# Kernel optimization log

Measured on AMD Instinct MI355X. Metric: run time of the kernel, lower is better.

## Reference

```python
import jax, jax.numpy as jnp
import numpy as np
from jax import lax

K = 3; KK = K * K; S = 1; P = 1; D = 1
BN_EPS = 1e-5


def setup_inputs() -> dict:
    key = jax.random.key(0)
    ks = jax.random.split(key, 4)
    B, C, H, W = 8, 128, 64, 64
    cout = 128
    # xavier-ish scales for conv weights
    def xavier(k, shape):
        fan_in = shape[1] * shape[2] * shape[3]
        fan_out = shape[0] * shape[2] * shape[3]
        limit = np.sqrt(6.0 / (fan_in + fan_out))
        return jax.random.uniform(k, shape, jnp.float32, -limit, limit)
    return {
        "x": jax.random.normal(ks[0], (B, C, H, W), jnp.float32),
        "w_off": xavier(ks[1], (2 * KK, C, K, K)),
        "b_off": jnp.zeros((2 * KK,), jnp.float32),
        "w_mod": xavier(ks[2], (KK, C, K, K)),
        "b_mod": jnp.zeros((KK,), jnp.float32),
        "w_reg": xavier(ks[3], (cout, C, K, K)),
        "b_reg": jnp.zeros((cout,), jnp.float32),
        "gamma": jnp.ones((cout,), jnp.float32),
        "beta": jnp.zeros((cout,), jnp.float32),
    }


def _conv(x, w, b):
    y = lax.conv_general_dilated(x, w, (S, S), [(P, P), (P, P)],
                                 rhs_dilation=(D, D),
                                 dimension_numbers=("NCHW", "OIHW", "NCHW"))
    return y + b[None, :, None, None]


def _deform_conv(x, offset, mask, w_reg, b_reg):
    B, C, H, W = x.shape
    Ho, Wo = offset.shape[2], offset.shape[3]
    # torchvision layout: [B, 2*KK, Ho, Wo], interleaved (dy, dx) per tap
    off = offset.reshape(B, KK, 2, Ho, Wo)
    dy, dx = off[:, :, 0], off[:, :, 1]                      # [B,KK,Ho,Wo]
    ki = jnp.arange(KK) // K
    kj = jnp.arange(KK) % K
    base_y = (jnp.arange(Ho) * S - P)[None, :, None] + (ki * D)[:, None, None]  # [KK,Ho,1]
    base_x = (jnp.arange(Wo) * S - P)[None, None, :] + (kj * D)[:, None, None]  # [KK,1,Wo]
    py = base_y[None].astype(x.dtype) + dy                   # [B,KK,Ho,Wo]
    px = base_x[None].astype(x.dtype) + dx

    y0f = jnp.floor(py); x0f = jnp.floor(px)
    ly = py - y0f; lx = px - x0f
    y0 = y0f.astype(jnp.int32); x0 = x0f.astype(jnp.int32)
    y1 = y0 + 1; x1 = x0 + 1

    def gather(iy, ix):
        valid = ((iy >= 0) & (iy < H) & (ix >= 0) & (ix < W)).astype(x.dtype)
        iyc = jnp.clip(iy, 0, H - 1)
        ixc = jnp.clip(ix, 0, W - 1)
        v = jax.vmap(lambda img, a, b: img[:, a, b])(x, iyc, ixc)  # [B,C,KK,Ho,Wo]
        return v * valid[:, None]

    val = (gather(y0, x0) * ((1 - ly) * (1 - lx))[:, None]
           + gather(y0, x1) * ((1 - ly) * lx)[:, None]
           + gather(y1, x0) * (ly * (1 - lx))[:, None]
           + gather(y1, x1) * (ly * lx)[:, None])               # [B,C,KK,Ho,Wo]

    patches = val * mask[:, None]                               # modulated samples
    wr = w_reg.reshape(w_reg.shape[0], C, KK)
    out = jnp.einsum("ock,bckhw->bohw", wr, patches)
    return out + b_reg[None, :, None, None]


def reference(x, w_off, b_off, w_mod, b_mod, w_reg, b_reg, gamma, beta):
    offset = _conv(x, w_off, b_off)
    modulator = 2.0 * jax.nn.sigmoid(_conv(x, w_mod, b_mod))
    y = _deform_conv(x, offset, modulator, w_reg, b_reg)
    # BatchNorm2d (training-mode batch statistics) + ReLU
    mu = y.mean(axis=(0, 2, 3), keepdims=True)
    var = y.var(axis=(0, 2, 3), keepdims=True)
    y = (y - mu) * lax.rsqrt(var + BN_EPS)
    y = y * gamma[None, :, None, None] + beta[None, :, None, None]
    return jax.nn.relu(y)
```

## Files before the change

### kernel.cpp

```cpp
#include <hip/hip_runtime.h>
#include <math.h>

#define H 64
#define W 64
#define C 128
#define NB 8
#define COUT 128
#define HWi 4096
#define NKC 36
#define PADu 40

typedef __attribute__((ext_vector_type(8))) short short8;
typedef __attribute__((ext_vector_type(8))) unsigned short ushort8;
typedef __attribute__((ext_vector_type(4))) unsigned short ushort4v;
typedef __attribute__((ext_vector_type(4))) float f32x4;

__device__ __forceinline__ unsigned short f2bf(float f){
    unsigned u = __float_as_uint(f);
    unsigned r = (u + 0x7FFFu + ((u >> 16) & 1u)) >> 16;
    return (unsigned short)r;
}
__device__ __forceinline__ float bf2f(unsigned short u){
    return __uint_as_float(((unsigned)u) << 16);
}

__global__ void k_pre(const float* __restrict__ x, unsigned short* __restrict__ xTp,
                      const float* __restrict__ w_reg, const float* __restrict__ w_off,
                      const float* __restrict__ w_mod, const float* __restrict__ b_off,
                      const float* __restrict__ b_mod,
                      unsigned short* __restrict__ wAv, unsigned short* __restrict__ w27A,
                      float* __restrict__ biasom, float* __restrict__ psum){
    int tid = threadIdx.x;
    if (blockIdx.x >= 528){
        int i = (blockIdx.x - 528) * 256 + tid;
        if (i < 147456){
            int kc = i >> 12, rem = i & 4095;
            int q = rem >> 10, r = (rem >> 3) & 127, j = rem & 7;
            int kk = kc * 32 + q * 8 + j, k = kk >> 7, c = kk & 127;
            wAv[i] = f2bf(w_reg[r * 1152 + c * 9 + k]);
        } else if (i < 147456 + 36864){
            int j2 = i - 147456;
            int kc = j2 >> 10, rem = j2 & 1023, m = rem >> 5, kkl = rem & 31;
            int kk = kc * 32 + kkl, k = kk >> 7, c = kk & 127;
            float v = 0.f;
            if (m < 18) v = w_off[m * 1152 + c * 9 + k];
            else if (m < 27) v = w_mod[(m - 18) * 1152 + c * 9 + k];
            w27A[j2] = f2bf(v);
        } else if (i < 147456 + 36864 + 32){
            int m = i - 147456 - 36864;
            biasom[m] = (m < 18) ? b_off[m] : (m < 27 ? b_mod[m - 18] : 0.f);
        } else if (i < 147456 + 36864 + 32 + 256){
            psum[i - 147456 - 36864 - 32] = 0.f;
        }
        return;
    }
    int bidx = blockIdx.x;
    int b = bidx & 7, hp = bidx >> 3;
    unsigned short* row = xTp + (size_t)(b * 66 + hp) * 66 * 128;
    if (hp == 0 || hp == 65){
        ushort8 z = {0,0,0,0,0,0,0,0};
        for (int i = tid; i < 66 * 128 / 8; i += 256) ((ushort8*)row)[i] = z;
        return;
    }
    int h = hp - 1;
    __shared__ unsigned short s[64 * 136];
    int w = tid & 63, c0 = tid >> 6;
    for (int cc = 0; cc < 128; cc += 4){
        int c = cc + c0;
        s[w * 136 + c] = f2bf(x[(size_t)(b * 128 + c) * HWi + h * 64 + w]);
    }
    __syncthreads();
    if (tid < 32){
        ushort8 z = {0,0,0,0,0,0,0,0};
        int wp = (tid < 16) ? 0 : 65;
        int sg = tid & 15;
        *(ushort8*)(row + wp * 128 + sg * 8) = z;
    }
    for (int it = tid; it < 1024; it += 256){
        int w2 = it >> 4, sg = it & 15;
        *(ushort8*)(row + (w2 + 1) * 128 + sg * 8) = *(const ushort8*)(s + w2 * 136 + sg * 8);
    }
}

__global__ __launch_bounds__(512, 4) void k_fused(const unsigned short* __restrict__ xTp,
        const unsigned short* __restrict__ w27A, const float* __restrict__ biasom,
        const unsigned short* __restrict__ wAv, const float* __restrict__ b_reg,
        unsigned short* __restrict__ ybf, float* __restrict__ psum){
    __shared__ char smem[79872];
    int tid = threadIdx.x;
    int lb = (blockIdx.x & 7) * 64 + (blockIdx.x >> 3);
    int n0 = lb * 64;
    int b = n0 >> 12, h = (n0 >> 6) & 63;

    {
        int grp = tid >> 8, gt = tid & 255;
        unsigned short* pA = (unsigned short*)(smem + grp * 15360);
        unsigned short* pB = (unsigned short*)(smem + grp * 15360 + 5120);
        int wvg = gt >> 6, lane = gt & 63, quad = lane >> 4, l16 = lane & 15;
        int nl = gt >> 2, sg = gt & 3;
        f32x4 acc0 = {0.f,0.f,0.f,0.f}, acc1 = {0.f,0.f,0.f,0.f};
        int kc0 = grp * 18;
        auto p1load = [&](int i, ushort8& A8, ushort8& B8){
            int kc = kc0 + i;
            int k = kc >> 2, cb = (kc & 3) << 5;
            int ki = k / 3, kj = k - ki * 3;
            if (gt < 128) A8 = *(const ushort8*)(w27A + kc * 1024 + gt * 8);
            int rowi = (b * 66 + h + ki) * 66 + (nl + kj);
            B8 = *(const ushort8*)(xTp + (size_t)rowi * 128 + cb + sg * 8);
        };
        auto p1body = [&](int i, ushort8& A8, ushort8& B8){
            int p = i & 1;
            if (gt < 128) *(ushort8*)(pA + p * 1280 + (gt >> 2) * PADu + (gt & 3) * 8) = A8;
            *(ushort8*)(pB + p * 2560 + nl * PADu + sg * 8) = B8;
            if (i + 2 < 18) p1load(i + 2, A8, B8);
            __syncthreads();
            short8 bfrag = *(const short8*)(pB + p * 2560 + (wvg * 16 + l16) * PADu + quad * 8);
            short8 a0 = *(const short8*)(pA + p * 1280 + l16 * PADu + quad * 8);
            short8 a1 = *(const short8*)(pA + p * 1280 + (16 + l16) * PADu + quad * 8);
            acc0 = __builtin_amdgcn_mfma_f32_16x16x32_bf16(a0, bfrag, acc0, 0, 0, 0);
            acc1 = __builtin_amdgcn_mfma_f32_16x16x32_bf16(a1, bfrag, acc1, 0, 0, 0);
        };
        ushort8 rA0, rB0, rA1, rB1;
        p1load(0, rA0, rB0);
        p1load(1, rA1, rB1);
        for (int ih = 0; ih < 9; ih++){
            p1body(ih * 2,     rA0, rB0);
            p1body(ih * 2 + 1, rA1, rB1);
        }
        float* s_red = (float*)(smem + 30720);
        int npx = wvg * 16 + l16;
        if (grp == 1){
            #pragma unroll
            for (int t = 0; t < 2; t++){
                f32x4 a = t ? acc1 : acc0;
                #pragma unroll
                for (int r = 0; r < 4; r++)
                    s_red[npx * 32 + t * 16 + quad * 4 + r] = a[r];
            }
        }
        __syncthreads();
        if (grp == 0){
            unsigned short* s_OM = (unsigned short*)smem;
            #pragma unroll
            for (int t = 0; t < 2; t++){
                f32x4 a = t ? acc1 : acc0;
                #pragma unroll
                for (int r = 0; r < 4; r++){
                    int oc = t * 16 + quad * 4 + r;
                    float v = a[r] + s_red[npx * 32 + oc] + biasom[oc];
                    if (oc >= 18) v = 2.f / (1.f + expf(-v));
                    s_OM[npx * 32 + oc] = f2bf(v);
                }
            }
        }
        __syncthreads();
    }

    unsigned short* sA = (unsigned short*)smem;
    unsigned short* sB = (unsigned short*)(smem + 40960);
    int*   s_a0 = (int*)(smem + 61440);
    float* s_w0 = (float*)(smem + 70656);
    const unsigned short* s_OM = (const unsigned short*)smem;

    for (int idx = tid; idx < 576; idx += 512){
        int k = idx >> 6, px_ = idx & 63;
        float dy = bf2f(s_OM[px_ * 32 + 2 * k]);
        float dx = bf2f(s_OM[px_ * 32 + 2 * k + 1]);
        float m  = bf2f(s_OM[px_ * 32 + 18 + k]);
        int ki = k / 3, kj = k - ki * 3;
        float py  = (float)(h - 1 + ki) + dy;
        float pxf = (float)(px_ - 1 + kj) + dx;
        float y0f = floorf(py), x0f = floorf(pxf);
        float ly = py - y0f, lx = pxf - x0f;
        int iy0 = (int)y0f, ix0 = (int)x0f;
        int cy0 = min(max(iy0 + 1, 0), 65), cy1 = min(max(iy0 + 2, 0), 65);
        int cx0 = min(max(ix0 + 1, 0), 65), cx1 = min(max(ix0 + 2, 0), 65);
        int rb = b * 66 * 66;
        s_a0[0 * 576 + idx] = ((rb + cy0 * 66) + cx0) * 128;
        s_a0[1 * 576 + idx] = ((rb + cy0 * 66) + cx1) * 128;
        s_a0[2 * 576 + idx] = ((rb + cy1 * 66) + cx0) * 128;
        s_a0[3 * 576 + idx] = ((rb + cy1 * 66) + cx1) * 128;
        s_w0[0 * 576 + idx] = (1.f - ly) * (1.f - lx) * m;
        s_w0[1 * 576 + idx] = (1.f - ly) * lx * m;
        s_w0[2 * 576 + idx] = ly * (1.f - lx) * m;
        s_w0[3 * 576 + idx] = ly * lx * m;
    }
    __syncthreads();

    int wv = tid >> 6, lane = tid & 63, quad = lane >> 4, l16 = lane & 15;
    int ocq = wv & 3, ng = wv >> 2;
    int rA = tid & 127, qA = tid >> 7;
    int cA = (qA ^ ((rA >> 3) & 3)) * 8;
    int px = tid >> 3, cg = tid & 7;

    int rowA0 = ocq * 32 + l16, rowA1 = rowA0 + 16;
    int offA0 = rowA0 * PADu + (quad ^ ((rowA0 >> 3) & 3)) * 8;
    int offA1 = rowA1 * PADu + (quad ^ ((rowA1 >> 3) & 3)) * 8;
    int offB0 = (ng * 32 + l16) * PADu + quad * 8;
    int offB1 = (ng * 32 + 16 + l16) * PADu + quad * 8;

    f32x4 acc00 = {0.f,0.f,0.f,0.f}, acc01 = {0.f,0.f,0.f,0.f};
    f32x4 acc10 = {0.f,0.f,0.f,0.f}, acc11 = {0.f,0.f,0.f,0.f};

    auto loadP = [&](int j, ushort8& W0, ushort8& W1, ushort8& C0, ushort8& C1,
                     ushort8& C2, ushort8& C3, float4& Wt){
        W0 = *(const ushort8*)(wAv + (size_t)(2 * j) * 4096 + tid * 8);
        W1 = *(const ushort8*)(wAv + (size_t)(2 * j + 1) * 4096 + tid * 8);
        int k = j >> 1, cb = (j & 1) << 6;
        int idx = k * 64 + px;
        int co = cb + cg * 8;
        Wt.x = s_w0[0 * 576 + idx]; Wt.y = s_w0[1 * 576 + idx];
        Wt.z = s_w0[2 * 576 + idx]; Wt.w = s_w0[3 * 576 + idx];
        C0 = *(const ushort8*)(xTp + s_a0[0 * 576 + idx] + co);
        C1 = *(const ushort8*)(xTp + s_a0[1 * 576 + idx] + co);
        C2 = *(const ushort8*)(xTp + s_a0[2 * 576 + idx] + co);
        C3 = *(const ushort8*)(xTp + s_a0[3 * 576 + idx] + co);
    };
    auto bodyP = [&](int j, ushort8& W0, ushort8& W1, ushort8& C0, ushort8& C1,
                     ushort8& C2, ushort8& C3, float4& Wt){
        int p = j & 1;
        unsigned short* sAp = sA + p * 10240;
        unsigned short* sBp = sB + p * 5120;
        *(ushort8*)(sAp + rA * PADu + cA) = W0;
        *(ushort8*)(sAp + 5120 + rA * PADu + cA) = W1;
        {
            ushort8 o;
            #pragma unroll
            for (int s = 0; s < 8; s++){
                float v = Wt.x * bf2f(C0[s]) + Wt.y * bf2f(C1[s])
                        + Wt.z * bf2f(C2[s]) + Wt.w * bf2f(C3[s]);
                o[s] = f2bf(v);
            }
            *(ushort8*)(sBp + (cg >> 2) * 2560 + px * PADu + (cg & 3) * 8) = o;
        }
        if (j + 2 < 18) loadP(j + 2, W0, W1, C0, C1, C2, C3, Wt);
        __syncthreads();
        #pragma unroll
        for (int u = 0; u < 2; u++){
            const unsigned short* A = sAp + u * 5120;
            const unsigned short* Bn = sBp + u * 2560;
            short8 a0 = *(const short8*)(A + offA0);
            short8 a1 = *(const short8*)(A + offA1);
            short8 b0 = *(const short8*)(Bn + offB0);
            short8 b1 = *(const short8*)(Bn + offB1);
            acc00 = __builtin_amdgcn_mfma_f32_16x16x32_bf16(a0, b0, acc00, 0, 0, 0);
            acc01 = __builtin_amdgcn_mfma_f32_16x16x32_bf16(a0, b1, acc01, 0, 0, 0);
            acc10 = __builtin_amdgcn_mfma_f32_16x16x32_bf16(a1, b0, acc10, 0, 0, 0);
            acc11 = __builtin_amdgcn_mfma_f32_16x16x32_bf16(a1, b1, acc11, 0, 0, 0);
        }
    };

    ushort8 W0a, W1a, C0a, C1a, C2a, C3a, W0b, W1b, C0b, C1b, C2b, C3b;
    float4 Wta, Wtb;
    loadP(0, W0a, W1a, C0a, C1a, C2a, C3a, Wta);
    loadP(1, W0b, W1b, C0b, C1b, C2b, C3b, Wtb);
    for (int jh = 0; jh < 9; jh++){
        bodyP(jh * 2,     W0a, W1a, C0a, C1a, C2a, C3a, Wta);
        bodyP(jh * 2 + 1, W0b, W1b, C0b, C1b, C2b, C3b, Wtb);
    }

    __syncthreads();
    float* ls = (float*)smem;
    int sp0 = h * 64;
    #pragma unroll
    for (int to = 0; to < 2; to++){
        #pragma unroll
        for (int tn = 0; tn < 2; tn++){
            f32x4 a = to ? (tn ? acc11 : acc10) : (tn ? acc01 : acc00);
            int nl = ng * 32 + tn * 16 + l16;
            #pragma unroll
            for (int r = 0; r < 4; r++){
                int oc = ocq * 32 + to * 16 + quad * 4 + r;
                float v = a[r] + b_reg[oc];
                ybf[(size_t)(b * 128 + oc) * HWi + sp0 + nl] = f2bf(v);
                ls[oc * 67 + nl] = v;
            }
        }
    }
    __syncthreads();
    if (tid < 128){
        int oc = tid;
        float s = 0.f, s2 = 0.f;
        #pragma unroll 8
        for (int nl = 0; nl < 64; nl++){
            float v = ls[oc * 67 + nl];
            s += v; s2 = fmaf(v, v, s2);
        }
        atomicAdd(&psum[oc], s);
        atomicAdd(&psum[128 + oc], s2);
    }
}

__global__ void k_apply(const unsigned short* __restrict__ ybf, const float* __restrict__ psum,
                        const float* __restrict__ gamma, const float* __restrict__ beta,
                        float* __restrict__ out){
    int lb = ((int)blockIdx.x & 7) * 256 + ((int)blockIdx.x >> 3);
    int e8 = (lb * 256 + (int)threadIdx.x) * 8;
    int c = (e8 >> 12) & 127;
    ushort8 u = *(const ushort8*)(ybf + e8);
    float s = psum[c], s2 = psum[128 + c];
    float mean = s * (1.f / 32768.f);
    float var  = s2 * (1.f / 32768.f) - mean * mean;
    float rs = rsqrtf(var + 1e-5f);
    float g = gamma[c] * rs;
    float bt = beta[c] - mean * g;
    float4 lo, hi;
    lo.x = fmaxf(fmaf(bf2f(u[0]), g, bt), 0.f);
    lo.y = fmaxf(fmaf(bf2f(u[1]), g, bt), 0.f);
    lo.z = fmaxf(fmaf(bf2f(u[2]), g, bt), 0.f);
    lo.w = fmaxf(fmaf(bf2f(u[3]), g, bt), 0.f);
    hi.x = fmaxf(fmaf(bf2f(u[4]), g, bt), 0.f);
    hi.y = fmaxf(fmaf(bf2f(u[5]), g, bt), 0.f);
    hi.z = fmaxf(fmaf(bf2f(u[6]), g, bt), 0.f);
    hi.w = fmaxf(fmaf(bf2f(u[7]), g, bt), 0.f);
    *(float4*)(out + e8)     = lo;
    *(float4*)(out + e8 + 4) = hi;
}

extern "C" void kernel_launch(void* const* d_in, const int* in_sizes, int n_in,
                              void* d_out, int out_size, void* d_ws, size_t ws_size,
                              hipStream_t stream){
    const float* x     = (const float*)d_in[0];
    const float* w_off = (const float*)d_in[1];
    const float* b_off = (const float*)d_in[2];
    const float* w_mod = (const float*)d_in[3];
    const float* b_mod = (const float*)d_in[4];
    const float* w_reg = (const float*)d_in[5];
    const float* b_reg = (const float*)d_in[6];
    const float* gamma = (const float*)d_in[7];
    const float* beta  = (const float*)d_in[8];

    char* wsb = (char*)d_ws;
    unsigned short* xTp   = (unsigned short*)(wsb);
    unsigned short* ybf   = (unsigned short*)(wsb + 11018240);
    unsigned short* wAv   = (unsigned short*)(wsb + 19406848);
    unsigned short* w27A  = (unsigned short*)(wsb + 19701760);
    float*          biasom= (float*)(wsb + 19775488);
    float*          psum  = (float*)(wsb + 19775616);
    float* out = (float*)d_out;

    hipLaunchKernelGGL(k_pre,   dim3(1250), dim3(256), 0, stream, x, xTp, w_reg, w_off, w_mod, b_off, b_mod, wAv, w27A, biasom, psum);
    hipLaunchKernelGGL(k_fused, dim3(512),  dim3(512), 0, stream, xTp, w27A, biasom, wAv, b_reg, ybf, psum);
    hipLaunchKernelGGL(k_apply, dim3(2048), dim3(256), 0, stream, ybf, psum, gamma, beta, out);
}
```

Measured before the change: 132.4 us.

## Load MFMA weight fragments directly from global, dropping LDS staging for weights

Both GEMM phases now read their A-operand weight fragments straight from global memory into registers, with the weight pre-layout changed so each lane's fragment is contiguous. This removes the LDS round trip for weights and cuts shared memory from about 78KB to 38KB, which could allow more resident blocks. The bf16 packing of the bilinear samples now uses the hardware v_cvt_pk_bf16_f32 instruction. In exchange, weight loads happen every iteration with global latency that is no longer prefetched two stages ahead, and these loads rely on L2/L1 hits since every block re-reads the weights.

```diff
diff --git a/kernel.cpp b/kernel.cpp
--- a/kernel.cpp
+++ b/kernel.cpp
@@ -12,7 +12,7 @@
 
 typedef __attribute__((ext_vector_type(8))) short short8;
 typedef __attribute__((ext_vector_type(8))) unsigned short ushort8;
-typedef __attribute__((ext_vector_type(4))) unsigned short ushort4v;
+typedef __attribute__((ext_vector_type(4))) unsigned int uint4v;
 typedef __attribute__((ext_vector_type(4))) float f32x4;
 
 __device__ __forceinline__ unsigned short f2bf(float f){
@@ -22,6 +22,11 @@
 }
 __device__ __forceinline__ float bf2f(unsigned short u){
     return __uint_as_float(((unsigned)u) << 16);
+}
+__device__ __forceinline__ unsigned cvtpk_bf16(float lo, float hi){
+    unsigned r;
+    asm("v_cvt_pk_bf16_f32 %0, %1, %2" : "=v"(r) : "v"(lo), "v"(hi));
+    return r;
 }
 
 __global__ void k_pre(const float* __restrict__ x, unsigned short* __restrict__ xTp,
@@ -40,7 +45,9 @@
             wAv[i] = f2bf(w_reg[r * 1152 + c * 9 + k]);
         } else if (i < 147456 + 36864){
             int j2 = i - 147456;
-            int kc = j2 >> 10, rem = j2 & 1023, m = rem >> 5, kkl = rem & 31;
+            int kc = j2 >> 10, rem = j2 & 1023;
+            int q = rem >> 8, m = (rem >> 3) & 31, t = rem & 7;
+            int kkl = q * 8 + t;
             int kk = kc * 32 + kkl, k = kk >> 7, c = kk & 127;
             float v = 0.f;
             if (m < 18) v = w_off[m * 1152 + c * 9 + k];
@@ -86,7 +93,7 @@
         const unsigned short* __restrict__ w27A, const float* __restrict__ biasom,
         const unsigned short* __restrict__ wAv, const float* __restrict__ b_reg,
         unsigned short* __restrict__ ybf, float* __restrict__ psum){
-    __shared__ char smem[79872];
+    __shared__ char smem[38912];
     int tid = threadIdx.x;
     int lb = (blockIdx.x & 7) * 64 + (blockIdx.x >> 3);
     int n0 = lb * 64;
@@ -94,40 +101,39 @@
 
     {
         int grp = tid >> 8, gt = tid & 255;
-        unsigned short* pA = (unsigned short*)(smem + grp * 15360);
-        unsigned short* pB = (unsigned short*)(smem + grp * 15360 + 5120);
+        unsigned short* pB = (unsigned short*)(smem + grp * 10240);
         int wvg = gt >> 6, lane = gt & 63, quad = lane >> 4, l16 = lane & 15;
         int nl = gt >> 2, sg = gt & 3;
         f32x4 acc0 = {0.f,0.f,0.f,0.f}, acc1 = {0.f,0.f,0.f,0.f};
         int kc0 = grp * 18;
-        auto p1load = [&](int i, ushort8& A8, ushort8& B8){
+        auto p1load = [&](int i, ushort8& B8){
             int kc = kc0 + i;
             int k = kc >> 2, cb = (kc & 3) << 5;
             int ki = k / 3, kj = k - ki * 3;
-            if (gt < 128) A8 = *(const ushort8*)(w27A + kc * 1024 + gt * 8);
             int rowi = (b * 66 + h + ki) * 66 + (nl + kj);
             B8 = *(const ushort8*)(xTp + (size_t)rowi * 128 + cb + sg * 8);
         };
-        auto p1body = [&](int i, ushort8& A8, ushort8& B8){
+        auto p1body = [&](int i, ushort8& B8){
             int p = i & 1;
-            if (gt < 128) *(ushort8*)(pA + p * 1280 + (gt >> 2) * PADu + (gt & 3) * 8) = A8;
+            int kc = kc0 + i;
+            const unsigned short* wj = w27A + kc * 1024 + quad * 256;
+            short8 a0 = *(const short8*)(wj + l16 * 8);
+            short8 a1 = *(const short8*)(wj + (16 + l16) * 8);
             *(ushort8*)(pB + p * 2560 + nl * PADu + sg * 8) = B8;
-            if (i + 2 < 18) p1load(i + 2, A8, B8);
+            if (i + 2 < 18) p1load(i + 2, B8);
             __syncthreads();
             short8 bfrag = *(const short8*)(pB + p * 2560 + (wvg * 16 + l16) * PADu + quad * 8);
-            short8 a0 = *(const short8*)(pA + p * 1280 + l16 * PADu + quad * 8);
-            short8 a1 = *(const short8*)(pA + p * 1280 + (16 + l16) * PADu + quad * 8);
             acc0 = __builtin_amdgcn_mfma_f32_16x16x32_bf16(a0, bfrag, acc0, 0, 0, 0);
             acc1 = __builtin_amdgcn_mfma_f32_16x16x32_bf16(a1, bfrag, acc1, 0, 0, 0);
         };
-        ushort8 rA0, rB0, rA1, rB1;
-        p1load(0, rA0, rB0);
-        p1load(1, rA1, rB1);
+        ushort8 rB0, rB1;
+        p1load(0, rB0);
+        p1load(1, rB1);
         for (int ih = 0; ih < 9; ih++){
-            p1body(ih * 2,     rA0, rB0);
-            p1body(ih * 2 + 1, rA1, rB1);
-        }
-        float* s_red = (float*)(smem + 30720);
+            p1body(ih * 2,     rB0);
+            p1body(ih * 2 + 1, rB1);
+        }
+        float* s_red = (float*)(smem + 20480);
         int npx = wvg * 16 + l16;
         if (grp == 1){
             #pragma unroll
@@ -156,10 +162,9 @@
         __syncthreads();
     }
 
-    unsigned short* sA = (unsigned short*)smem;
-    unsigned short* sB = (unsigned short*)(smem + 40960);
-    int*   s_a0 = (int*)(smem + 61440);
-    float* s_w0 = (float*)(smem + 70656);
+    unsigned short* sB = (unsigned short*)smem;
+    int*   s_a0 = (int*)(smem + 20480);
+    float* s_w0 = (float*)(smem + 29696);
     const unsigned short* s_OM = (const unsigned short*)smem;
 
     for (int idx = tid; idx < 576; idx += 512){
@@ -189,23 +194,16 @@
 
     int wv = tid >> 6, lane = tid & 63, quad = lane >> 4, l16 = lane & 15;
     int ocq = wv & 3, ng = wv >> 2;
-    int rA = tid & 127, qA = tid >> 7;
-    int cA = (qA ^ ((rA >> 3) & 3)) * 8;
     int px = tid >> 3, cg = tid & 7;
 
     int rowA0 = ocq * 32 + l16, rowA1 = rowA0 + 16;
-    int offA0 = rowA0 * PADu + (quad ^ ((rowA0 >> 3) & 3)) * 8;
-    int offA1 = rowA1 * PADu + (quad ^ ((rowA1 >> 3) & 3)) * 8;
     int offB0 = (ng * 32 + l16) * PADu + quad * 8;
     int offB1 = (ng * 32 + 16 + l16) * PADu + quad * 8;
 
     f32x4 acc00 = {0.f,0.f,0.f,0.f}, acc01 = {0.f,0.f,0.f,0.f};
     f32x4 acc10 = {0.f,0.f,0.f,0.f}, acc11 = {0.f,0.f,0.f,0.f};
 
-    auto loadP = [&](int j, ushort8& W0, ushort8& W1, ushort8& C0, ushort8& C1,
-                     ushort8& C2, ushort8& C3, float4& Wt){
-        W0 = *(const ushort8*)(wAv + (size_t)(2 * j) * 4096 + tid * 8);
-        W1 = *(const ushort8*)(wAv + (size_t)(2 * j + 1) * 4096 + tid * 8);
+    auto loadP = [&](int j, ushort8& C0, ushort8& C1, ushort8& C2, ushort8& C3, float4& Wt){
         int k = j >> 1, cb = (j & 1) << 6;
         int idx = k * 64 + px;
         int co = cb + cg * 8;
@@ -216,47 +214,47 @@
         C2 = *(const ushort8*)(xTp + s_a0[2 * 576 + idx] + co);
         C3 = *(const ushort8*)(xTp + s_a0[3 * 576 + idx] + co);
     };
-    auto bodyP = [&](int j, ushort8& W0, ushort8& W1, ushort8& C0, ushort8& C1,
-                     ushort8& C2, ushort8& C3, float4& Wt){
+    auto bodyP = [&](int j, ushort8& C0, ushort8& C1, ushort8& C2, ushort8& C3, float4& Wt){
         int p = j & 1;
-        unsigned short* sAp = sA + p * 10240;
         unsigned short* sBp = sB + p * 5120;
-        *(ushort8*)(sAp + rA * PADu + cA) = W0;
-        *(ushort8*)(sAp + 5120 + rA * PADu + cA) = W1;
-        {
-            ushort8 o;
-            #pragma unroll
-            for (int s = 0; s < 8; s++){
-                float v = Wt.x * bf2f(C0[s]) + Wt.y * bf2f(C1[s])
-                        + Wt.z * bf2f(C2[s]) + Wt.w * bf2f(C3[s]);
-                o[s] = f2bf(v);
-            }
-            *(ushort8*)(sBp + (cg >> 2) * 2560 + px * PADu + (cg & 3) * 8) = o;
-        }
-        if (j + 2 < 18) loadP(j + 2, W0, W1, C0, C1, C2, C3, Wt);
+        const unsigned short* wj = wAv + (size_t)(2 * j) * 4096 + quad * 1024;
+        short8 a00 = *(const short8*)(wj + rowA0 * 8);
+        short8 a01 = *(const short8*)(wj + rowA1 * 8);
+        short8 a10 = *(const short8*)(wj + 4096 + rowA0 * 8);
+        short8 a11 = *(const short8*)(wj + 4096 + rowA1 * 8);
+        uint4v ov;
+        #pragma unroll
+        for (int q = 0; q < 4; q++){
+            float v0 = Wt.x * bf2f(C0[2*q])   + Wt.y * bf2f(C1[2*q])
+                     + Wt.z * bf2f(C2[2*q])   + Wt.w * bf2f(C3[2*q]);
+            float v1 = Wt.x * bf2f(C0[2*q+1]) + Wt.y * bf2f(C1[2*q+1])
+                     + Wt.z * bf2f(C2[2*q+1]) + Wt.w * bf2f(C3[2*q+1]);
+            ov[q] = cvtpk_bf16(v0, v1);
+        }
+        *(uint4v*)(sBp + (cg >> 2) * 2560 + px * PADu + (cg & 3) * 8) = ov;
+        if (j + 2 < 18) loadP(j + 2, C0, C1, C2, C3, Wt);
         __syncthreads();
-        #pragma unroll
-        for (int u = 0; u < 2; u++){
-            const unsigned short* A = sAp + u * 5120;
-            const unsigned short* Bn = sBp + u * 2560;
-            short8 a0 = *(const short8*)(A + offA0);
-            short8 a1 = *(const short8*)(A + offA1);
-            short8 b0 = *(const short8*)(Bn + offB0);
-            short8 b1 = *(const short8*)(Bn + offB1);
-            acc00 = __builtin_amdgcn_mfma_f32_16x16x32_bf16(a0, b0, acc00, 0, 0, 0);
-            acc01 = __builtin_amdgcn_mfma_f32_16x16x32_bf16(a0, b1, acc01, 0, 0, 0);
-            acc10 = __builtin_amdgcn_mfma_f32_16x16x32_bf16(a1, b0, acc10, 0, 0, 0);
-            acc11 = __builtin_amdgcn_mfma_f32_16x16x32_bf16(a1, b1, acc11, 0, 0, 0);
-        }
+        short8 b0 = *(const short8*)(sBp + offB0);
+        short8 b1 = *(const short8*)(sBp + offB1);
+        acc00 = __builtin_amdgcn_mfma_f32_16x16x32_bf16(a00, b0, acc00, 0, 0, 0);
+        acc01 = __builtin_amdgcn_mfma_f32_16x16x32_bf16(a00, b1, acc01, 0, 0, 0);
+        acc10 = __builtin_amdgcn_mfma_f32_16x16x32_bf16(a01, b0, acc10, 0, 0, 0);
+        acc11 = __builtin_amdgcn_mfma_f32_16x16x32_bf16(a01, b1, acc11, 0, 0, 0);
+        b0 = *(const short8*)(sBp + 2560 + offB0);
+        b1 = *(const short8*)(sBp + 2560 + offB1);
+        acc00 = __builtin_amdgcn_mfma_f32_16x16x32_bf16(a10, b0, acc00, 0, 0, 0);
+        acc01 = __builtin_amdgcn_mfma_f32_16x16x32_bf16(a10, b1, acc01, 0, 0, 0);
+        acc10 = __builtin_amdgcn_mfma_f32_16x16x32_bf16(a11, b0, acc10, 0, 0, 0);
+        acc11 = __builtin_amdgcn_mfma_f32_16x16x32_bf16(a11, b1, acc11, 0, 0, 0);
     };
 
-    ushort8 W0a, W1a, C0a, C1a, C2a, C3a, W0b, W1b, C0b, C1b, C2b, C3b;
+    ushort8 C0a, C1a, C2a, C3a, C0b, C1b, C2b, C3b;
     float4 Wta, Wtb;
-    loadP(0, W0a, W1a, C0a, C1a, C2a, C3a, Wta);
-    loadP(1, W0b, W1b, C0b, C1b, C2b, C3b, Wtb);
+    loadP(0, C0a, C1a, C2a, C3a, Wta);
+    loadP(1, C0b, C1b, C2b, C3b, Wtb);
     for (int jh = 0; jh < 9; jh++){
-        bodyP(jh * 2,     W0a, W1a, C0a, C1a, C2a, C3a, Wta);
-        bodyP(jh * 2 + 1, W0b, W1b, C0b, C1b, C2b, C3b, Wtb);
+        bodyP(jh * 2,     C0a, C1a, C2a, C3a, Wta);
+        bodyP(jh * 2 + 1, C0b, C1b, C2b, C3b, Wtb);
     }
 
     __syncthreads();
```

New measurement: 130.3 us. Within noise of the previous version (-1.6%).
